# Performance work log

Measured on AMD Instinct MI355X. Metric: run time of the kernel, lower is better.

The kernel has to match this reference:

```python
import jax, jax.numpy as jnp
import numpy as np

B, S, D, H = 4, 1024, 1024, 16
DH = D // H  # head_dim = 64


def setup_inputs() -> dict:
    key = jax.random.key(0)
    kq, kk, kv, kl, kwq, kwk, kwv, kwo = jax.random.split(key, 8)
    query = jax.random.normal(kq, (B, S, D), dtype=jnp.float32)
    key_t = jax.random.normal(kk, (B, S, D), dtype=jnp.float32)
    value = jax.random.normal(kv, (B, S, D), dtype=jnp.float32)
    # padding: keys at positions >= valid length are padded (True)
    lengths = jax.random.randint(kl, (B,), S // 2, S + 1)
    key_padding_mask = jnp.arange(S)[None, :] >= lengths[:, None]  # [B,S] bool
    scale = 1.0 / np.sqrt(D)
    Wq = jax.random.normal(kwq, (D, D), dtype=jnp.float32) * scale
    Wk = jax.random.normal(kwk, (D, D), dtype=jnp.float32) * scale
    Wv = jax.random.normal(kwv, (D, D), dtype=jnp.float32) * scale
    Wo = jax.random.normal(kwo, (D, D), dtype=jnp.float32) * scale
    gamma = jnp.ones((H,), dtype=jnp.float32)
    return {"query": query, "key": key_t, "value": value,
            "key_padding_mask": key_padding_mask,
            "Wq": Wq, "Wk": Wk, "Wv": Wv, "Wo": Wo, "gamma": gamma}


def reference(query, key, value, key_padding_mask, Wq, Wk, Wv, Wo, gamma):
    # nn.Linear(x) = x @ W.T (bias=False)
    q = jnp.einsum('bsd,ed->bse', query, Wq).reshape(B, S, H, DH).transpose(0, 2, 1, 3)  # [B,H,S,Dh]
    k = jnp.einsum('bsd,ed->bse', key, Wk).reshape(B, S, H, DH).transpose(0, 2, 1, 3)
    v = jnp.einsum('bsd,ed->bse', value, Wv).reshape(B, S, H, DH).transpose(0, 2, 1, 3)
    scores = jnp.einsum('bhqd,bhkd->bhqk', q, k) / jnp.sqrt(jnp.float32(DH))
    pad = key_padding_mask[:, None, None, :]  # [B,1,1,S]
    scores = jnp.where(pad, -jnp.inf, scores)
    v = jnp.where(key_padding_mask[:, None, :, None], 0.0, v)
    attn = jax.nn.softmax(scores, axis=-1)  # dropout p=0 (eval) -> identity
    ws = jnp.einsum('bhqk,bhkd->bhqd', attn, v)
    ws = ws * gamma[None, :, None, None]  # per-head scale
    ws = ws.transpose(0, 2, 1, 3).reshape(B, S, D)
    return jnp.einsum('bsd,ed->bse', ws, Wo)
```

## Files before the change

### kernel.cpp

```cpp
#include <hip/hip_runtime.h>
#include <math.h>

#define S_LEN 1024
#define DMODEL 1024

typedef __attribute__((ext_vector_type(8))) short bf16x8;
typedef __attribute__((ext_vector_type(4))) short bf16x4;
typedef __attribute__((ext_vector_type(4))) float f32x4;

#define MFMA16(a, b, c) __builtin_amdgcn_mfma_f32_16x16x32_bf16(a, b, c, 0, 0, 0)

#define WP (1024u * 1024u)
#define XP (4u * 1024u * 1024u)

__device__ __forceinline__ unsigned short rne_bf16(float f) {
    unsigned u = __float_as_uint(f);
    u += 0x7FFFu + ((u >> 16) & 1u);
    return (unsigned short)(u >> 16);
}

__device__ __forceinline__ void split_rne(float f, unsigned short& h, unsigned short& l) {
    unsigned short hh = rne_bf16(f);
    float lf = f - __uint_as_float(((unsigned)hh) << 16);
    h = hh;
    l = rne_bf16(lf);
}

typedef const __attribute__((address_space(1))) unsigned int* gas_t;
typedef __attribute__((address_space(3))) unsigned int* las_t;
__device__ __forceinline__ void glds16(const void* g, void* l) {
    __builtin_amdgcn_global_load_lds((gas_t)g, (las_t)l, 16, 0, 0);
}

__global__ __launch_bounds__(256)
void convert_wx(const float* __restrict__ W0, const float* __restrict__ W1,
                const float* __restrict__ W2, const float* __restrict__ W3,
                const float* __restrict__ Xq, const float* __restrict__ Xk,
                const float* __restrict__ Xv,
                unsigned short* __restrict__ Wpl, unsigned short* __restrict__ Xbase) {
    int blk = blockIdx.x;
    if (blk < 4096) {
        const int which = blk >> 10;
        const float* W = which == 0 ? W0 : which == 1 ? W1 : which == 2 ? W2 : W3;
        int i = ((blk & 1023) * 256 + threadIdx.x) * 4;
        float4 f = *(const float4*)&W[i];
        if (which == 3) {
            unsigned short* hi = Wpl + 3 * WP;
            unsigned short* lo = Wpl + 4 * WP;
            bf16x4 h, l;
            unsigned short hh, ll;
            split_rne(f.x, hh, ll); h[0] = (short)hh; l[0] = (short)ll;
            split_rne(f.y, hh, ll); h[1] = (short)hh; l[1] = (short)ll;
            split_rne(f.z, hh, ll); h[2] = (short)hh; l[2] = (short)ll;
            split_rne(f.w, hh, ll); h[3] = (short)hh; l[3] = (short)ll;
            *(bf16x4*)&hi[i] = h;
            *(bf16x4*)&lo[i] = l;
        } else {
            unsigned short* hi = Wpl + (size_t)which * WP;
            bf16x4 h;
            h[0] = (short)rne_bf16(f.x);
            h[1] = (short)rne_bf16(f.y);
            h[2] = (short)rne_bf16(f.z);
            h[3] = (short)rne_bf16(f.w);
            *(bf16x4*)&hi[i] = h;
        }
    } else {
        blk -= 4096;
        const int which = blk >> 12;
        const float* X = which == 0 ? Xq : which == 1 ? Xk : Xv;
        unsigned short* Xr = Xbase + (size_t)which * XP;
        int i = ((blk & 4095) * 256 + threadIdx.x) * 4;
        float4 f = *(const float4*)&X[i];
        bf16x4 h;
        h[0] = (short)rne_bf16(f.x);
        h[1] = (short)rne_bf16(f.y);
        h[2] = (short)rne_bf16(f.z);
        h[3] = (short)rne_bf16(f.w);
        *(bf16x4*)&Xr[i] = h;
    }
}

__global__ __launch_bounds__(256)
void gemm_proj(const unsigned short* __restrict__ Xbase,
               const unsigned short* __restrict__ Wpl,
               unsigned short* __restrict__ Obase) {
    __shared__ unsigned short AS[128 * 32];
    __shared__ unsigned short BS[128 * 32];

    const int z = blockIdx.z;
    const unsigned short* A = Xbase + (size_t)z * XP;
    const unsigned short* B = Wpl + (size_t)z * WP;

    const int t = threadIdx.x, lane = t & 63, w = t >> 6;
    const int quad = lane >> 4, l15 = lane & 15;
    const int wr = w & 1, wc = w >> 1;

    const int linb = blockIdx.x + (blockIdx.y << 3);
    const int swz = ((linb & 7) << 5) + (linb >> 3);
    const int bx = swz & 7, by = swz >> 3;
    const int rowBase = by * 128, colBase = bx * 128;

    const unsigned short* gA[2];
    const unsigned short* gB[2];
    unsigned short* lA[2];
    unsigned short* lB[2];
    #pragma unroll
    for (int e = 0; e < 2; e++) {
        int row = w * 32 + e * 16 + (lane >> 2);
        int cg = (lane & 3) ^ ((row >> 1) & 3);
        gA[e] = A + (size_t)(rowBase + row) * 1024 + cg * 8;
        gB[e] = B + (size_t)(colBase + row) * 1024 + cg * 8;
        lA[e] = &AS[(w * 32 + e * 16) * 32];
        lB[e] = &BS[(w * 32 + e * 16) * 32];
    }

    int aAd[4], bAd[4];
    #pragma unroll
    for (int i = 0; i < 4; i++) {
        int ra = wr * 64 + i * 16 + l15;
        aAd[i] = ra * 32 + (quad ^ ((ra >> 1) & 3)) * 8;
        int rb = wc * 64 + i * 16 + l15;
        bAd[i] = rb * 32 + (quad ^ ((rb >> 1) & 3)) * 8;
    }

    f32x4 acc[4][4] = {};

    for (int kt = 0; kt < 32; kt++) {
        if (kt) __syncthreads();
        const int ko = kt * 32;
        glds16(gA[0] + ko, lA[0]);
        glds16(gA[1] + ko, lA[1]);
        glds16(gB[0] + ko, lB[0]);
        glds16(gB[1] + ko, lB[1]);
        __syncthreads();

        bf16x8 af[4], bfr[4];
        #pragma unroll
        for (int i = 0; i < 4; i++) af[i] = *(const bf16x8*)&AS[aAd[i]];
        #pragma unroll
        for (int j = 0; j < 4; j++) bfr[j] = *(const bf16x8*)&BS[bAd[j]];
        #pragma unroll
        for (int j = 0; j < 4; j++)
            #pragma unroll
            for (int i = 0; i < 4; i++)
                acc[i][j] = MFMA16(af[i], bfr[j], acc[i][j]);
    }

    unsigned short* O = Obase + (size_t)z * XP;
    #pragma unroll
    for (int i = 0; i < 4; i++)
        #pragma unroll
        for (int j = 0; j < 4; j++)
            #pragma unroll
            for (int r = 0; r < 4; r++) {
                int m = rowBase + wr * 64 + i * 16 + quad * 4 + r;
                int n = colBase + wc * 64 + j * 16 + l15;
                int bb = m >> 10, s = m & 1023, hh = n >> 6, dh = n & 63;
                size_t hb = ((size_t)(bb * 16 + hh)) << 16;
                unsigned short v = rne_bf16(acc[i][j][r]);
                if (z == 2) O[hb + (size_t)dh * 1024 + s] = v;
                else        O[hb + s * 64 + dh] = v;
            }
}

__global__ __launch_bounds__(256)
void gemm_out2(const unsigned short* __restrict__ A,
               const unsigned short* __restrict__ Bh, const unsigned short* __restrict__ Bl,
               float* __restrict__ Cf) {
    __shared__ unsigned short AS[128 * 32];
    __shared__ unsigned short BhS[64 * 32], BlS[64 * 32];

    const int t = threadIdx.x, lane = t & 63, w = t >> 6;
    const int quad = lane >> 4, l15 = lane & 15;
    const int wr = w & 1, wc = w >> 1;

    const int linb = blockIdx.x + (blockIdx.y << 4);
    const int swz = ((linb & 7) << 6) + (linb >> 3);
    const int bx = swz & 15, by = swz >> 4;
    const int rowBase = by * 128, colBase = bx * 64;

    const unsigned short* gA[2];
    unsigned short* lA[2];
    #pragma unroll
    for (int e = 0; e < 2; e++) {
        int row = w * 32 + e * 16 + (lane >> 2);
        int cg = (lane & 3) ^ ((row >> 1) & 3);
        gA[e] = A + (size_t)(rowBase + row) * 1024 + cg * 8;
        lA[e] = &AS[(w * 32 + e * 16) * 32];
    }
    const unsigned short *gBh, *gBl;
    unsigned short *lBh, *lBl;
    {
        int row = w * 16 + (lane >> 2);
        int cg = (lane & 3) ^ ((row >> 1) & 3);
        gBh = Bh + (size_t)(colBase + row) * 1024 + cg * 8;
        gBl = Bl + (size_t)(colBase + row) * 1024 + cg * 8;
        lBh = &BhS[(w * 16) * 32];
        lBl = &BlS[(w * 16) * 32];
    }

    int aAd[4], bAd[2];
    #pragma unroll
    for (int i = 0; i < 4; i++) {
        int ra = wr * 64 + i * 16 + l15;
        aAd[i] = ra * 32 + (quad ^ ((ra >> 1) & 3)) * 8;
    }
    #pragma unroll
    for (int j = 0; j < 2; j++) {
        int rb = wc * 32 + j * 16 + l15;
        bAd[j] = rb * 32 + (quad ^ ((rb >> 1) & 3)) * 8;
    }

    f32x4 acc[4][2] = {};

    for (int kt = 0; kt < 32; kt++) {
        if (kt) __syncthreads();
        const int ko = kt * 32;
        glds16(gA[0] + ko, lA[0]);
        glds16(gA[1] + ko, lA[1]);
        glds16(gBh + ko, lBh);
        glds16(gBl + ko, lBl);
        __syncthreads();

        bf16x8 af[4], bhf[2], blf[2];
        #pragma unroll
        for (int i = 0; i < 4; i++) af[i] = *(const bf16x8*)&AS[aAd[i]];
        #pragma unroll
        for (int j = 0; j < 2; j++) {
            bhf[j] = *(const bf16x8*)&BhS[bAd[j]];
            blf[j] = *(const bf16x8*)&BlS[bAd[j]];
        }
        #pragma unroll
        for (int j = 0; j < 2; j++)
            #pragma unroll
            for (int i = 0; i < 4; i++) {
                acc[i][j] = MFMA16(af[i], bhf[j], acc[i][j]);
                acc[i][j] = MFMA16(af[i], blf[j], acc[i][j]);
            }
    }

    #pragma unroll
    for (int i = 0; i < 4; i++)
        #pragma unroll
        for (int j = 0; j < 2; j++)
            #pragma unroll
            for (int r = 0; r < 4; r++) {
                int m = rowBase + wr * 64 + i * 16 + quad * 4 + r;
                int n = colBase + wc * 32 + j * 16 + l15;
                Cf[(size_t)m * 1024 + n] = acc[i][j][r];
            }
}

__global__ __launch_bounds__(256)
void attn_mfma(const unsigned short* __restrict__ Qr, const unsigned short* __restrict__ Kr,
               const unsigned short* __restrict__ Vt,
               const int* __restrict__ mask, const float* __restrict__ gamma,
               unsigned short* __restrict__ WSr) {
    __shared__ int maskS[1024];
    __shared__ unsigned short Ks[64 * 72];
    __shared__ unsigned short Vs[64 * 72];
    __shared__ unsigned short Ph[4 * 16 * 72];

    const int t = threadIdx.x, lane = t & 63, w = t >> 6;
    const int quad = lane >> 4, l15 = lane & 15;

    const int linb = blockIdx.x + (blockIdx.y << 4);
    const int swz = ((linb & 7) << 5) + (linb >> 3);
    const int qx = swz & 15, h = swz >> 4;

    const int q0 = qx * 64, b = blockIdx.z;
    const size_t hb = ((size_t)(b * 16 + h)) << 16;

    ((int4*)maskS)[t] = ((const int4*)(mask + b * 1024))[t];

    bf16x8 qhi[2];
    {
        const int qrow = q0 + w * 16 + l15;
        const size_t qb = hb + (size_t)qrow * 64 + quad * 8;
        qhi[0] = *(const bf16x8*)&Qr[qb];
        qhi[1] = *(const bf16x8*)&Qr[qb + 32];
    }

    const int sc = (t & 7) * 8;
    const int sr = t >> 3;

    f32x4 o[4] = {};
    float lsum[4] = {0.f, 0.f, 0.f, 0.f};

    bf16x8 kreg[2], vreg[2];
    #pragma unroll
    for (int e = 0; e < 2; e++) {
        int row = e * 32 + sr;
        kreg[e] = *(const bf16x8*)&Kr[hb + (size_t)row * 64 + sc];
        vreg[e] = *(const bf16x8*)&Vt[hb + (size_t)row * 1024 + sc];
    }
    __syncthreads();
    #pragma unroll
    for (int e = 0; e < 2; e++) {
        int row = e * 32 + sr;
        *(bf16x8*)&Ks[row * 72 + sc] = kreg[e];
        *(bf16x8*)&Vs[row * 72 + sc] = vreg[e];
    }
    __syncthreads();

    for (int jt = 0; jt < 16; jt++) {
        const int j0 = jt * 64;
        if (maskS[j0]) break;
        const bool partial = maskS[j0 + 63] != 0;
        const int j0n = j0 + 64;
        const bool pf = (jt < 15) && (maskS[j0n] == 0);

        if (pf) {
            #pragma unroll
            for (int e = 0; e < 2; e++) {
                int row = e * 32 + sr;
                kreg[e] = *(const bf16x8*)&Kr[hb + (size_t)(j0n + row) * 64 + sc];
                vreg[e] = *(const bf16x8*)&Vt[hb + (size_t)row * 1024 + j0n + sc];
            }
        }

        f32x4 s4[4] = {};
        __builtin_amdgcn_s_setprio(1);
        #pragma unroll
        for (int nj = 0; nj < 4; nj++) {
            int kr = (nj * 16 + l15) * 72 + quad * 8;
            #pragma unroll
            for (int kk = 0; kk < 2; kk++) {
                bf16x8 kv = *(const bf16x8*)&Ks[kr + kk * 32];
                s4[nj] = MFMA16(qhi[kk], kv, s4[nj]);
            }
        }
        __builtin_amdgcn_s_setprio(0);

        if (partial) {
            #pragma unroll
            for (int nj = 0; nj < 4; nj++) {
                int mk = maskS[j0 + nj * 16 + l15];
                #pragma unroll
                for (int r = 0; r < 4; r++) {
                    float p = mk ? 0.f : __expf(s4[nj][r] * 0.125f);
                    lsum[r] += p;
                    Ph[(w * 16 + quad * 4 + r) * 72 + nj * 16 + l15] = rne_bf16(p);
                }
            }
        } else {
            #pragma unroll
            for (int nj = 0; nj < 4; nj++) {
                #pragma unroll
                for (int r = 0; r < 4; r++) {
                    float p = __expf(s4[nj][r] * 0.125f);
                    lsum[r] += p;
                    Ph[(w * 16 + quad * 4 + r) * 72 + nj * 16 + l15] = rne_bf16(p);
                }
            }
        }

        bf16x8 ph[2];
        #pragma unroll
        for (int ks = 0; ks < 2; ks++)
            ph[ks] = *(const bf16x8*)&Ph[(w * 16 + l15) * 72 + ks * 32 + quad * 8];
        __builtin_amdgcn_s_setprio(1);
        #pragma unroll
        for (int dt = 0; dt < 4; dt++) {
            int vr = (dt * 16 + l15) * 72 + quad * 8;
            #pragma unroll
            for (int ks = 0; ks < 2; ks++) {
                bf16x8 vv = *(const bf16x8*)&Vs[vr + ks * 32];
                o[dt] = MFMA16(ph[ks], vv, o[dt]);
            }
        }
        __builtin_amdgcn_s_setprio(0);

        if (pf) {
            __syncthreads();
            #pragma unroll
            for (int e = 0; e < 2; e++) {
                int row = e * 32 + sr;
                *(bf16x8*)&Ks[row * 72 + sc] = kreg[e];
                *(bf16x8*)&Vs[row * 72 + sc] = vreg[e];
            }
            __syncthreads();
        }
    }

    #pragma unroll
    for (int r = 0; r < 4; r++) {
        lsum[r] += __shfl_xor(lsum[r], 1);
        lsum[r] += __shfl_xor(lsum[r], 2);
        lsum[r] += __shfl_xor(lsum[r], 4);
        lsum[r] += __shfl_xor(lsum[r], 8);
    }

    const float g = gamma[h];
    #pragma unroll
    for (int r = 0; r < 4; r++) {
        const int qrow = q0 + w * 16 + quad * 4 + r;
        const float sc2 = g / lsum[r];
        const size_t base = ((size_t)b * 1024 + qrow) * 1024 + h * 64;
        #pragma unroll
        for (int dt = 0; dt < 4; dt++)
            WSr[base + dt * 16 + l15] = rne_bf16(o[dt][r] * sc2);
    }
}

extern "C" void kernel_launch(void* const* d_in, const int* in_sizes, int n_in,
                              void* d_out, int out_size, void* d_ws, size_t ws_size,
                              hipStream_t stream) {
    const float* query = (const float*)d_in[0];
    const float* key   = (const float*)d_in[1];
    const float* value = (const float*)d_in[2];
    const int*   mask  = (const int*)d_in[3];
    const float* Wq    = (const float*)d_in[4];
    const float* Wk    = (const float*)d_in[5];
    const float* Wv    = (const float*)d_in[6];
    const float* Wo    = (const float*)d_in[7];
    const float* gamma = (const float*)d_in[8];
    float* out = (float*)d_out;

    unsigned short* u = (unsigned short*)d_ws;
    unsigned short* Xbase = u;
    unsigned short* Obase = u + 3 * XP;
    unsigned short* Wpl   = u + 6 * XP;
    unsigned short* WSr   = Xbase;
    unsigned short* Qr = Obase, *Kr = Obase + XP, *Vt = Obase + 2 * XP;
    unsigned short* Woh = Wpl + 3 * WP, *Wol = Wpl + 4 * WP;

    convert_wx<<<16384, 256, 0, stream>>>(Wq, Wk, Wv, Wo, query, key, value, Wpl, Xbase);

    gemm_proj<<<dim3(8, 32, 3), 256, 0, stream>>>(Xbase, Wpl, Obase);

    attn_mfma<<<dim3(16, 16, 4), 256, 0, stream>>>(Qr, Kr, Vt, mask, gamma, WSr);

    gemm_out2<<<dim3(16, 32), 256, 0, stream>>>(WSr, Woh, Wol, out);
}
```

Measured before the change: 209.1 us.

## Skip K/V conversion and projection for fully padded key tiles

Convert and project K/V rows only where keys are not padded. Conversion skips padded rows whose 128-row tile starts padded, and zero-fills padded rows in partially padded tiles. The projection GEMM exits early for K/V tiles whose first row is masked, and the V-transpose store is vectorised into 4-element writes. This saves memory traffic and MFMA work on padded keys, but it relies on the attention kernel never reading the unwritten projected K/V for those tiles, which may be stale workspace.

```diff
diff --git a/kernel.cpp b/kernel.cpp
--- a/kernel.cpp
+++ b/kernel.cpp
@@ -36,7 +36,7 @@
 void convert_wx(const float* __restrict__ W0, const float* __restrict__ W1,
                 const float* __restrict__ W2, const float* __restrict__ W3,
                 const float* __restrict__ Xq, const float* __restrict__ Xk,
-                const float* __restrict__ Xv,
+                const float* __restrict__ Xv, const int* __restrict__ mask,
                 unsigned short* __restrict__ Wpl, unsigned short* __restrict__ Xbase) {
     int blk = blockIdx.x;
     if (blk < 4096) {
@@ -70,6 +70,15 @@
         const float* X = which == 0 ? Xq : which == 1 ? Xk : Xv;
         unsigned short* Xr = Xbase + (size_t)which * XP;
         int i = ((blk & 4095) * 256 + threadIdx.x) * 4;
+        if (which != 0) {
+            const int b = i >> 20, s = (i >> 10) & 1023;
+            if (mask[b * 1024 + s]) {
+                if (mask[b * 1024 + (s & ~127)]) return;
+                bf16x4 zz = {0, 0, 0, 0};
+                *(bf16x4*)&Xr[i] = zz;
+                return;
+            }
+        }
         float4 f = *(const float4*)&X[i];
         bf16x4 h;
         h[0] = (short)rne_bf16(f.x);
@@ -83,6 +92,7 @@
 __global__ __launch_bounds__(256)
 void gemm_proj(const unsigned short* __restrict__ Xbase,
                const unsigned short* __restrict__ Wpl,
+               const int* __restrict__ mask,
                unsigned short* __restrict__ Obase) {
     __shared__ unsigned short AS[128 * 32];
     __shared__ unsigned short BS[128 * 32];
@@ -99,6 +109,8 @@
     const int swz = ((linb & 7) << 5) + (linb >> 3);
     const int bx = swz & 7, by = swz >> 3;
     const int rowBase = by * 128, colBase = bx * 128;
+
+    if (z && mask[(by >> 3) * 1024 + ((by & 7) << 7)]) return;
 
     const unsigned short* gA[2];
     const unsigned short* gB[2];
@@ -150,17 +162,22 @@
     #pragma unroll
     for (int i = 0; i < 4; i++)
         #pragma unroll
-        for (int j = 0; j < 4; j++)
-            #pragma unroll
-            for (int r = 0; r < 4; r++) {
-                int m = rowBase + wr * 64 + i * 16 + quad * 4 + r;
-                int n = colBase + wc * 64 + j * 16 + l15;
-                int bb = m >> 10, s = m & 1023, hh = n >> 6, dh = n & 63;
-                size_t hb = ((size_t)(bb * 16 + hh)) << 16;
-                unsigned short v = rne_bf16(acc[i][j][r]);
-                if (z == 2) O[hb + (size_t)dh * 1024 + s] = v;
-                else        O[hb + s * 64 + dh] = v;
-            }
+        for (int j = 0; j < 4; j++) {
+            const int m0 = rowBase + wr * 64 + i * 16 + quad * 4;
+            const int n = colBase + wc * 64 + j * 16 + l15;
+            const int bb = m0 >> 10, s = m0 & 1023, hh = n >> 6, dh = n & 63;
+            const size_t hb = ((size_t)(bb * 16 + hh)) << 16;
+            if (z == 2) {
+                bf16x4 v4;
+                #pragma unroll
+                for (int r = 0; r < 4; r++) v4[r] = (short)rne_bf16(acc[i][j][r]);
+                *(bf16x4*)&O[hb + (size_t)dh * 1024 + s] = v4;
+            } else {
+                #pragma unroll
+                for (int r = 0; r < 4; r++)
+                    O[hb + (size_t)(s + r) * 64 + dh] = rne_bf16(acc[i][j][r]);
+            }
+        }
 }
 
 __global__ __launch_bounds__(256)
@@ -425,9 +442,9 @@
     unsigned short* Qr = Obase, *Kr = Obase + XP, *Vt = Obase + 2 * XP;
     unsigned short* Woh = Wpl + 3 * WP, *Wol = Wpl + 4 * WP;
 
-    convert_wx<<<16384, 256, 0, stream>>>(Wq, Wk, Wv, Wo, query, key, value, Wpl, Xbase);
-
-    gemm_proj<<<dim3(8, 32, 3), 256, 0, stream>>>(Xbase, Wpl, Obase);
+    convert_wx<<<16384, 256, 0, stream>>>(Wq, Wk, Wv, Wo, query, key, value, mask, Wpl, Xbase);
+
+    gemm_proj<<<dim3(8, 32, 3), 256, 0, stream>>>(Xbase, Wpl, mask, Obase);
 
     attn_mfma<<<dim3(16, 16, 4), 256, 0, stream>>>(Qr, Kr, Vt, mask, gamma, WSr);
 
```

After: 202.5 us. 1.03x faster.
